# Kernel optimization log

Hardware: AMD Instinct MI355X
Metric: run time of the kernel (lower is better)

## Reference

```python
import jax, jax.numpy as jnp
import numpy as np

B, S, H = 4, 2048, 1024
E, F = 8, 4096
K = 2  # hardcoded top-k in the original forward


def setup_inputs() -> dict:
    key = jax.random.key(0)
    ks = jax.random.split(key, 8)
    scale = 0.02
    x = jax.random.normal(ks[0], (B, S, H), dtype=jnp.float32)
    Wr = jax.random.normal(ks[1], (H, E), dtype=jnp.float32) * scale
    br = jnp.zeros((E,), dtype=jnp.float32)
    W1 = jax.random.normal(ks[2], (E, H, F), dtype=jnp.float32) * scale
    b1 = jnp.zeros((E, F), dtype=jnp.float32)
    W2 = jax.random.normal(ks[3], (E, F, H), dtype=jnp.float32) * scale
    b2 = jnp.zeros((E, H), dtype=jnp.float32)
    return {"x": x, "Wr": Wr, "br": br, "W1": W1, "b1": b1, "W2": W2, "b2": b2}


def reference(x, Wr, br, W1, b1, W2, b2):
    # Router: [B,S,H] @ [H,E] -> [B,S,E]
    router_logits = jnp.einsum('bsh,he->bse', x, Wr) + br
    router_probs = jax.nn.softmax(router_logits, axis=-1)
    top_k_probs, top_k_indices = jax.lax.top_k(router_probs, K)
    top_k_probs = top_k_probs / jnp.sum(top_k_probs, axis=-1, keepdims=True)
    # NOTE: original code weights EVERY selected expert by the normalized top-1 prob.
    p0 = top_k_probs[..., 0]  # [B,S]

    combined = jnp.zeros((B, S, H), dtype=x.dtype)
    for e in range(E):
        mask = jnp.any(top_k_indices == e, axis=-1)  # [B,S]
        # Dense FFN (dropout deterministic => identity); gelu approximate (flax default)
        h = jax.nn.gelu(jnp.einsum('bsh,hf->bsf', x, W1[e]) + b1[e])
        y = jnp.einsum('bsf,fh->bsh', h, W2[e]) + b2[e]
        combined = combined + jnp.where(mask[..., None], y * p0[..., None], 0.0)
    return combined
```

## Files before the change

kernel.cpp:

```cpp
#include <hip/hip_runtime.h>
#include <hip/hip_bf16.h>


typedef __bf16 bf16;
typedef __attribute__((ext_vector_type(4))) __bf16 bf16x4;
typedef __attribute__((ext_vector_type(8))) __bf16 bf16x8;
typedef __attribute__((ext_vector_type(4))) float f32x4;

#define GLD16(g, l) __builtin_amdgcn_global_load_lds( \
    (__attribute__((address_space(1))) void*)(g),      \
    (__attribute__((address_space(3))) void*)(l), 16, 0, 0)

__device__ __forceinline__ float gelu_fast(float v) {
  float u = v * fmaf(v * v, 0.0713548162726f, 1.5957691216057308f);
  return v * __builtin_amdgcn_rcpf(1.0f + __expf(-u));
}

__global__ __launch_bounds__(256) void router_kernel(
    const float* __restrict__ x, const float* __restrict__ Wr,
    const float* __restrict__ br, int* __restrict__ e01,
    float* __restrict__ p0arr) {
  int wv = threadIdx.x >> 6;
  int l = threadIdx.x & 63;
  int t = blockIdx.x * 4 + wv;
  float acc[8];
#pragma unroll
  for (int e = 0; e < 8; e++) acc[e] = 0.f;
  const float* xr = x + (size_t)t * 1024;
#pragma unroll
  for (int i = 0; i < 16; i++) {
    int h = l + i * 64;
    float xv = xr[h];
    const float4* w4 = (const float4*)(Wr + h * 8);
    float4 wa = w4[0], wb = w4[1];
    acc[0] += xv * wa.x; acc[1] += xv * wa.y; acc[2] += xv * wa.z; acc[3] += xv * wa.w;
    acc[4] += xv * wb.x; acc[5] += xv * wb.y; acc[6] += xv * wb.z; acc[7] += xv * wb.w;
  }
#pragma unroll
  for (int e = 0; e < 8; e++) {
    float v = acc[e];
#pragma unroll
    for (int m = 1; m < 64; m <<= 1) v += __shfl_xor(v, m, 64);
    acc[e] = v + br[e];
  }
  int i1 = 0; float m1 = acc[0];
#pragma unroll
  for (int e = 1; e < 8; e++) { if (acc[e] > m1) { m1 = acc[e]; i1 = e; } }
  int i2 = -1; float m2 = -3.4e38f;
#pragma unroll
  for (int e = 0; e < 8; e++) { if (e != i1 && acc[e] > m2) { m2 = acc[e]; i2 = e; } }
  if (l == 0) {
    e01[t] = i1 | (i2 << 8);
    p0arr[t] = 1.0f / (1.0f + __expf(m2 - m1));
  }
}

__global__ __launch_bounds__(1024) void slots_kernel(
    const int* __restrict__ e01, int* __restrict__ off,
    int* __restrict__ slot1, int* __restrict__ slot2) {
  __shared__ int wtot[16];
  int tid = threadIdx.x;
  int l = tid & 63, wv = tid >> 6;
  int t0 = tid * 8;
  int i1[8], i2[8];
#pragma unroll
  for (int i = 0; i < 8; i++) {
    int ee = e01[t0 + i];
    i1[i] = ee & 255;
    i2[i] = (ee >> 8) & 255;
  }
  int running = 0;
  for (int e = 0; e < 8; e++) {
    int cthread = 0;
#pragma unroll
    for (int i = 0; i < 8; i++) cthread += (i1[i] == e) + (i2[i] == e);
    int inc = cthread;
#pragma unroll
    for (int d = 1; d < 64; d <<= 1) {
      int v = __shfl_up(inc, d, 64);
      if (l >= d) inc += v;
    }
    if (l == 63) wtot[wv] = inc;
    __syncthreads();
    int wbase = 0, total = 0;
#pragma unroll
    for (int w = 0; w < 16; w++) {
      int tw = wtot[w];
      wbase += (w < wv) ? tw : 0;
      total += tw;
    }
    int base = running + wbase + (inc - cthread);
#pragma unroll
    for (int i = 0; i < 8; i++) {
      if (i1[i] == e) { slot1[t0 + i] = base; base++; }
      if (i2[i] == e) { slot2[t0 + i] = base; base++; }
    }
    if (tid == 0) off[e] = running;
    running += (total + 127) & ~127;
    __syncthreads();
  }
  if (tid == 0) off[8] = running;
}

__global__ __launch_bounds__(256) void gather_kernel(
    const float* __restrict__ x, const int* __restrict__ slot1,
    const int* __restrict__ slot2, bf16* __restrict__ Xg) {
  int t = blockIdx.x;
  int s1 = slot1[t], s2 = slot2[t];
  float4 v = ((const float4*)(x + (size_t)t * 1024))[threadIdx.x];
  bf16x4 bv = { (bf16)v.x, (bf16)v.y, (bf16)v.z, (bf16)v.w };
  *(bf16x4*)(Xg + (size_t)s1 * 1024 + threadIdx.x * 4) = bv;
  *(bf16x4*)(Xg + (size_t)s2 * 1024 + threadIdx.x * 4) = bv;
}

__global__ __launch_bounds__(256) void tconv_kernel(
    const float* __restrict__ in, bf16* __restrict__ out, int R, int C) {
  __shared__ float tile[64][65];
  size_t base = (size_t)blockIdx.z * R * C;
  int gr0 = blockIdx.y * 64, gc0 = blockIdx.x * 64;
#pragma unroll
  for (int i = 0; i < 16; i++) {
    int idx = threadIdx.x + i * 256;
    int r = idx >> 6, c = idx & 63;
    tile[r][c] = in[base + (size_t)(gr0 + r) * C + gc0 + c];
  }
  __syncthreads();
  int rr0 = (threadIdx.x & 15) * 4;
#pragma unroll
  for (int i = 0; i < 4; i++) {
    int cc = (threadIdx.x >> 4) + i * 16;
    bf16x4 v = { (bf16)tile[rr0][cc], (bf16)tile[rr0 + 1][cc],
                 (bf16)tile[rr0 + 2][cc], (bf16)tile[rr0 + 3][cc] };
    *(bf16x4*)&out[base + (size_t)(gc0 + cc) * R + gr0 + rr0] = v;
  }
}

__device__ __forceinline__ void gemm8_mainloop(
    const bf16* __restrict__ Abase, const bf16* __restrict__ Bbase,
    int K, char* smem, f32x4 acc[4][4], int wr, int wc, int l) {
  const int NT = K >> 6;
  int tid = threadIdx.x;
  size_t K2 = (size_t)K * 2;
  const char* sA0; const char* sA1;
  const char* sB0; const char* sB1; const char* sB2; const char* sB3;
  {
    int p0 = tid * 16, r0 = p0 >> 7, c0 = p0 & 127;
    int p1 = p0 + 8192, r1 = p1 >> 7, c1 = p1 & 127;
    int p2 = p0 + 16384, r2 = p2 >> 7, c2 = p2 & 127;
    int p3 = p0 + 24576, r3 = p3 >> 7, c3 = p3 & 127;
    sA0 = (const char*)Abase + (size_t)r0 * K2 + (c0 ^ ((r0 & 7) << 4));
    sA1 = (const char*)Abase + (size_t)r1 * K2 + (c1 ^ ((r1 & 7) << 4));
    sB0 = (const char*)Bbase + (size_t)r0 * K2 + (c0 ^ ((r0 & 7) << 4));
    sB1 = (const char*)Bbase + (size_t)r1 * K2 + (c1 ^ ((r1 & 7) << 4));
    sB2 = (const char*)Bbase + (size_t)r2 * K2 + (c2 ^ ((r2 & 7) << 4));
    sB3 = (const char*)Bbase + (size_t)r3 * K2 + (c3 ^ ((r3 & 7) << 4));
  }
  const int dA = tid * 16;
  const int dB = 16384 + tid * 16;
  int offA[4], offBf[4];
#pragma unroll
  for (int t = 0; t < 4; t++) {
    int ra = wr * 64 + t * 16 + (l & 15);
    offA[t] = ra * 128 + ((((l >> 4) << 4)) ^ ((ra & 7) << 4));
    int rb = wc * 64 + t * 16 + (l & 15);
    offBf[t] = 16384 + rb * 128 + ((((l >> 4) << 4)) ^ ((rb & 7) << 4));
  }
#pragma unroll
  for (int t = 0; t < 2; t++) {
    char* bu = smem + t * 49152;
    GLD16(sA0 + t * 128, bu + dA);
    GLD16(sA1 + t * 128, bu + dA + 8192);
    GLD16(sB0 + t * 128, bu + dB);
    GLD16(sB1 + t * 128, bu + dB + 8192);
    GLD16(sB2 + t * 128, bu + dB + 16384);
    GLD16(sB3 + t * 128, bu + dB + 24576);
  }
  sA0 += 256; sA1 += 256; sB0 += 256; sB1 += 256; sB2 += 256; sB3 += 256;
  asm volatile("s_waitcnt vmcnt(6)" ::: "memory");
  __builtin_amdgcn_s_barrier();
  char* bc = smem;
  char* bn2 = smem + 2 * 49152;
  for (int kt = 0; kt < NT; kt++) {
    bool st = (kt + 2) < NT;
    bf16x8 af[4], bfv[4];
#pragma unroll
    for (int t = 0; t < 4; t++) {
      af[t] = *(const bf16x8*)(bc + offA[t]);
      bfv[t] = *(const bf16x8*)(bc + offBf[t]);
    }
    if (st) {
      GLD16(sA0, bn2 + dA);
      GLD16(sA1, bn2 + dA + 8192);
      GLD16(sB0, bn2 + dB);
    }
    __builtin_amdgcn_s_barrier();
    asm volatile("s_waitcnt lgkmcnt(0)" ::: "memory");
    __builtin_amdgcn_s_setprio(1);
#pragma unroll
    for (int mf = 0; mf < 4; mf++)
#pragma unroll
      for (int nf = 0; nf < 4; nf++)
        acc[mf][nf] = __builtin_amdgcn_mfma_f32_16x16x32_bf16(bfv[nf], af[mf], acc[mf][nf], 0, 0, 0);
    __builtin_amdgcn_s_setprio(0);
    __builtin_amdgcn_s_barrier();
#pragma unroll
    for (int t = 0; t < 4; t++) {
      af[t] = *(const bf16x8*)(bc + (offA[t] ^ 64));
      bfv[t] = *(const bf16x8*)(bc + (offBf[t] ^ 64));
    }
    if (st) {
      GLD16(sB1, bn2 + dB + 8192);
      GLD16(sB2, bn2 + dB + 16384);
      GLD16(sB3, bn2 + dB + 24576);
      sA0 += 128; sA1 += 128; sB0 += 128; sB1 += 128; sB2 += 128; sB3 += 128;
    }
    __builtin_amdgcn_s_barrier();
    asm volatile("s_waitcnt lgkmcnt(0)" ::: "memory");
    __builtin_amdgcn_s_setprio(1);
#pragma unroll
    for (int mf = 0; mf < 4; mf++)
#pragma unroll
      for (int nf = 0; nf < 4; nf++)
        acc[mf][nf] = __builtin_amdgcn_mfma_f32_16x16x32_bf16(bfv[nf], af[mf], acc[mf][nf], 0, 0, 0);
    __builtin_amdgcn_s_setprio(0);
    if (st) {
      asm volatile("s_waitcnt vmcnt(6)" ::: "memory");
    } else if (kt + 1 < NT) {
      asm volatile("s_waitcnt vmcnt(0)" ::: "memory");
    }
    __builtin_amdgcn_s_barrier();
    bc += 49152; if (bc == smem + 147456) bc = smem;
    bn2 += 49152; if (bn2 == smem + 147456) bn2 = smem;
  }
}

__global__ __launch_bounds__(512) void gemm1_kernel(
    const bf16* __restrict__ Xg, const bf16* __restrict__ W1t,
    const float* __restrict__ b1, bf16* __restrict__ hbuf,
    const int* __restrict__ off) {
  __shared__ __align__(16) char smem[147456];
  int b = blockIdx.x;
  int xcd = b & 7, j = b >> 3;
  int m_tile = xcd * 17 + (j >> 4);
  int n_tile = j & 15;
  int row0 = m_tile * 128;
  if (row0 >= off[8]) return;
  int e = 0;
#pragma unroll
  for (int i = 0; i < 8; i++) { if (row0 >= off[i + 1]) e = i + 1; }
  int tid = threadIdx.x;
  int w = tid >> 6, l = tid & 63;
  int wr = w >> 2, wc = w & 3;
  f32x4 acc[4][4];
#pragma unroll
  for (int a = 0; a < 4; a++)
#pragma unroll
    for (int bb = 0; bb < 4; bb++) acc[a][bb] = (f32x4){0.f, 0.f, 0.f, 0.f};
  gemm8_mainloop(Xg + (size_t)row0 * 1024,
                 W1t + ((size_t)e * 4096 + n_tile * 256) * 1024,
                 1024, smem, acc, wr, wc, l);
  int mrow = l & 15, nq = (l >> 4) * 4;
  int gn0 = n_tile * 256 + wc * 64 + nq;
  f32x4 bv[4];
#pragma unroll
  for (int nf = 0; nf < 4; nf++)
    bv[nf] = *(const f32x4*)(b1 + e * 4096 + gn0 + nf * 16);
#pragma unroll
  for (int mf = 0; mf < 4; mf++) {
    int gm = row0 + wr * 64 + mf * 16 + mrow;
    bf16* rp = hbuf + (size_t)gm * 4096 + gn0;
#pragma unroll
    for (int nf = 0; nf < 4; nf++) {
      bf16x4 o;
#pragma unroll
      for (int jj = 0; jj < 4; jj++)
        o[jj] = (bf16)gelu_fast(acc[mf][nf][jj] + bv[nf][jj]);
      *(bf16x4*)(rp + nf * 16) = o;
    }
  }
}

__global__ __launch_bounds__(512) void gemm2_kernel(
    const bf16* __restrict__ hbuf, const bf16* __restrict__ W2t,
    const float* __restrict__ b2, bf16* __restrict__ yb,
    const int* __restrict__ off) {
  __shared__ __align__(16) char smem[147456];
  int b = blockIdx.x;
  int xcd = b & 7, j = b >> 3;
  int m_tile = xcd * 17 + (j >> 2);
  int n_tile = j & 3;
  int row0 = m_tile * 128;
  if (row0 >= off[8]) return;
  int e = 0;
#pragma unroll
  for (int i = 0; i < 8; i++) { if (row0 >= off[i + 1]) e = i + 1; }
  int tid = threadIdx.x;
  int w = tid >> 6, l = tid & 63;
  int wr = w >> 2, wc = w & 3;
  f32x4 acc[4][4];
#pragma unroll
  for (int a = 0; a < 4; a++)
#pragma unroll
    for (int bb = 0; bb < 4; bb++) acc[a][bb] = (f32x4){0.f, 0.f, 0.f, 0.f};
  gemm8_mainloop(hbuf + (size_t)row0 * 4096,
                 W2t + ((size_t)e * 1024 + n_tile * 256) * 4096,
                 4096, smem, acc, wr, wc, l);
  int mrow = l & 15, nq = (l >> 4) * 4;
  int gn0 = n_tile * 256 + wc * 64 + nq;
  f32x4 bv[4];
#pragma unroll
  for (int nf = 0; nf < 4; nf++)
    bv[nf] = *(const f32x4*)(b2 + e * 1024 + gn0 + nf * 16);
#pragma unroll
  for (int mf = 0; mf < 4; mf++) {
    int gm = row0 + wr * 64 + mf * 16 + mrow;
    bf16* rp = yb + (size_t)gm * 1024 + gn0;
#pragma unroll
    for (int nf = 0; nf < 4; nf++) {
      bf16x4 o;
#pragma unroll
      for (int jj = 0; jj < 4; jj++)
        o[jj] = (bf16)(acc[mf][nf][jj] + bv[nf][jj]);
      *(bf16x4*)(rp + nf * 16) = o;
    }
  }
}

__global__ __launch_bounds__(256) void combine_kernel(
    const bf16* __restrict__ yb, const int* __restrict__ slot1,
    const int* __restrict__ slot2, const float* __restrict__ p0arr,
    float* __restrict__ out) {
  int t = blockIdx.x;
  int s1 = slot1[t], s2 = slot2[t];
  float w0 = p0arr[t];
  bf16x4 a = *(const bf16x4*)(yb + (size_t)s1 * 1024 + threadIdx.x * 4);
  bf16x4 b = *(const bf16x4*)(yb + (size_t)s2 * 1024 + threadIdx.x * 4);
  float4 o;
  o.x = w0 * ((float)a[0] + (float)b[0]);
  o.y = w0 * ((float)a[1] + (float)b[1]);
  o.z = w0 * ((float)a[2] + (float)b[2]);
  o.w = w0 * ((float)a[3] + (float)b[3]);
  *(float4*)(out + (size_t)t * 1024 + threadIdx.x * 4) = o;
}

extern "C" void kernel_launch(void* const* d_in, const int* in_sizes, int n_in,
                              void* d_out, int out_size, void* d_ws, size_t ws_size,
                              hipStream_t stream) {
  const float* x  = (const float*)d_in[0];
  const float* Wr = (const float*)d_in[1];
  const float* br = (const float*)d_in[2];
  const float* W1 = (const float*)d_in[3];
  const float* b1 = (const float*)d_in[4];
  const float* W2 = (const float*)d_in[5];
  const float* b2 = (const float*)d_in[6];
  float* out = (float*)d_out;

  char* ws = (char*)d_ws;
  int*   off   = (int*)(ws + 0);
  int*   e01   = (int*)(ws + 256);
  float* p0    = (float*)(ws + 33024);
  int*   slot1 = (int*)(ws + 65792);
  int*   slot2 = (int*)(ws + 98560);
  bf16*  Xg    = (bf16*)(ws + 131584);
  bf16*  W1t   = (bf16*)(ws + 35783168ULL);
  bf16*  W2t   = (bf16*)(ws + 102892032ULL);
  bf16*  hb    = (bf16*)(ws + 170000896ULL);
  bf16*  yb    = Xg;

  tconv_kernel<<<dim3(64, 16, 8), 256, 0, stream>>>(W1, W1t, 1024, 4096);
  tconv_kernel<<<dim3(16, 64, 8), 256, 0, stream>>>(W2, W2t, 4096, 1024);
  router_kernel<<<2048, 256, 0, stream>>>(x, Wr, br, e01, p0);
  slots_kernel<<<1, 1024, 0, stream>>>(e01, off, slot1, slot2);
  gather_kernel<<<8192, 256, 0, stream>>>(x, slot1, slot2, Xg);
  gemm1_kernel<<<2176, 512, 0, stream>>>(Xg, W1t, b1, hb, off);
  gemm2_kernel<<<544, 512, 0, stream>>>(hb, W2t, b2, yb, off);
  combine_kernel<<<8192, 256, 0, stream>>>(yb, slot1, slot2, p0, out);
}
```

Before: 758.2 us.

## Use 256x256 expert GEMM tiles with per-expert tile list and 4-stage pipeline

Replaces the 128x256 GEMM tile with a 256x256 tile (8x4 MFMA fragments per wave) using a 64-wide K step and a 4-buffer, 3-ahead global-to-LDS prefetch ring. Experts are no longer padded to 128 rows. The slots kernel builds a compact list of 256-row tiles, each tagged with its expert, and the GEMMs mask stores past the expert's row end. Bigger tiles raise arithmetic intensity and halve the block count, at the cost of more accumulator registers and wasted MFMA work on partial tiles. The launch bounds request two blocks per CU.

```diff
diff --git a/kernel.cpp b/kernel.cpp
--- a/kernel.cpp
+++ b/kernel.cpp
@@ -56,7 +56,7 @@
 }
 
 __global__ __launch_bounds__(1024) void slots_kernel(
-    const int* __restrict__ e01, int* __restrict__ off,
+    const int* __restrict__ e01, int* __restrict__ meta,
     int* __restrict__ slot1, int* __restrict__ slot2) {
   __shared__ int wtot[16];
   int tid = threadIdx.x;
@@ -69,8 +69,10 @@
     i1[i] = ee & 255;
     i2[i] = (ee >> 8) & 255;
   }
+  int offl[9];
   int running = 0;
   for (int e = 0; e < 8; e++) {
+    offl[e] = running;
     int cthread = 0;
 #pragma unroll
     for (int i = 0; i < 8; i++) cthread += (i1[i] == e) + (i2[i] == e);
@@ -95,11 +97,19 @@
       if (i1[i] == e) { slot1[t0 + i] = base; base++; }
       if (i2[i] == e) { slot2[t0 + i] = base; base++; }
     }
-    if (tid == 0) off[e] = running;
-    running += (total + 127) & ~127;
+    running += total;
     __syncthreads();
   }
-  if (tid == 0) off[8] = running;
+  offl[8] = running;
+  if (tid == 0) {
+#pragma unroll
+    for (int e = 0; e < 9; e++) meta[e] = offl[e];
+    int nt = 0;
+    for (int e = 0; e < 8; e++)
+      for (int r = offl[e]; r < offl[e + 1]; r += 256)
+        meta[16 + (nt++)] = r | (e << 20);
+    meta[10] = nt;
+  }
 }
 
 __global__ __launch_bounds__(256) void gather_kernel(
@@ -135,63 +145,60 @@
   }
 }
 
-__device__ __forceinline__ void gemm8_mainloop(
+__device__ __forceinline__ void gemm256_core(
     const bf16* __restrict__ Abase, const bf16* __restrict__ Bbase,
-    int K, char* smem, f32x4 acc[4][4], int wr, int wc, int l) {
-  const int NT = K >> 6;
+    int K, int NT, char* smem, f32x4 acc[8][4], int wr, int wc, int l) {
   int tid = threadIdx.x;
   size_t K2 = (size_t)K * 2;
-  const char* sA0; const char* sA1;
-  const char* sB0; const char* sB1; const char* sB2; const char* sB3;
-  {
-    int p0 = tid * 16, r0 = p0 >> 7, c0 = p0 & 127;
-    int p1 = p0 + 8192, r1 = p1 >> 7, c1 = p1 & 127;
-    int p2 = p0 + 16384, r2 = p2 >> 7, c2 = p2 & 127;
-    int p3 = p0 + 24576, r3 = p3 >> 7, c3 = p3 & 127;
-    sA0 = (const char*)Abase + (size_t)r0 * K2 + (c0 ^ ((r0 & 7) << 4));
-    sA1 = (const char*)Abase + (size_t)r1 * K2 + (c1 ^ ((r1 & 7) << 4));
-    sB0 = (const char*)Bbase + (size_t)r0 * K2 + (c0 ^ ((r0 & 7) << 4));
-    sB1 = (const char*)Bbase + (size_t)r1 * K2 + (c1 ^ ((r1 & 7) << 4));
-    sB2 = (const char*)Bbase + (size_t)r2 * K2 + (c2 ^ ((r2 & 7) << 4));
-    sB3 = (const char*)Bbase + (size_t)r3 * K2 + (c3 ^ ((r3 & 7) << 4));
-  }
-  const int dA = tid * 16;
-  const int dB = 16384 + tid * 16;
-  int offA[4], offBf[4];
-#pragma unroll
-  for (int t = 0; t < 4; t++) {
-    int ra = wr * 64 + t * 16 + (l & 15);
-    offA[t] = ra * 128 + ((((l >> 4) << 4)) ^ ((ra & 7) << 4));
-    int rb = wc * 64 + t * 16 + (l & 15);
-    offBf[t] = 16384 + rb * 128 + ((((l >> 4) << 4)) ^ ((rb & 7) << 4));
-  }
-#pragma unroll
-  for (int t = 0; t < 2; t++) {
-    char* bu = smem + t * 49152;
-    GLD16(sA0 + t * 128, bu + dA);
-    GLD16(sA1 + t * 128, bu + dA + 8192);
-    GLD16(sB0 + t * 128, bu + dB);
-    GLD16(sB1 + t * 128, bu + dB + 8192);
-    GLD16(sB2 + t * 128, bu + dB + 16384);
-    GLD16(sB3 + t * 128, bu + dB + 24576);
-  }
-  sA0 += 256; sA1 += 256; sB0 += 256; sB1 += 256; sB2 += 256; sB3 += 256;
-  asm volatile("s_waitcnt vmcnt(6)" ::: "memory");
+  const char* src[4];
+  int dst[4];
+#pragma unroll
+  for (int i = 0; i < 4; i++) {
+    int s = (i & 1) ? (tid + 512) : tid;
+    int byteoff = s * 16;
+    int p = byteoff >> 7;
+    int W = byteoff & 127;
+    int L = W ^ ((p & 7) << 4);
+    int r = 2 * p + (L >> 6);
+    int c = L & 63;
+    const char* base = (const char*)((i >= 2) ? Bbase : Abase);
+    src[i] = base + (size_t)r * K2 + c;
+    dst[i] = ((i >= 2) ? 16384 : 0) + byteoff;
+  }
+  int offA[8], offB[4];
+  int kc16 = (l >> 4) << 4;
+#pragma unroll
+  for (int mf = 0; mf < 8; mf++) {
+    int r = wr * 128 + mf * 16 + (l & 15);
+    int p = r >> 1;
+    offA[mf] = (p << 7) + ((((r & 1) << 6) | kc16) ^ ((p & 7) << 4));
+  }
+#pragma unroll
+  for (int nf = 0; nf < 4; nf++) {
+    int r = wc * 64 + nf * 16 + (l & 15);
+    int p = r >> 1;
+    offB[nf] = 16384 + (p << 7) + ((((r & 1) << 6) | kc16) ^ ((p & 7) << 4));
+  }
+#pragma unroll
+  for (int t = 0; t < 3; t++) {
+    char* bu = smem + t * 32768;
+#pragma unroll
+    for (int i = 0; i < 4; i++) GLD16(src[i] + t * 64, bu + dst[i]);
+  }
+  asm volatile("s_waitcnt vmcnt(8)" ::: "memory");
   __builtin_amdgcn_s_barrier();
-  char* bc = smem;
-  char* bn2 = smem + 2 * 49152;
-  for (int kt = 0; kt < NT; kt++) {
-    bool st = (kt + 2) < NT;
-    bf16x8 af[4], bfv[4];
-#pragma unroll
-    for (int t = 0; t < 4; t++) {
-      af[t] = *(const bf16x8*)(bc + offA[t]);
-      bfv[t] = *(const bf16x8*)(bc + offBf[t]);
-    }
+  for (int t = 0; t < NT; t++) {
+    char* bc = smem + (t & 3) * 32768;
+    char* bs = smem + ((t + 3) & 3) * 32768;
+    bool st = (t + 3) < NT;
+    bf16x8 bfr[4], af[4];
+#pragma unroll
+    for (int nf = 0; nf < 4; nf++) bfr[nf] = *(const bf16x8*)(bc + offB[nf]);
+#pragma unroll
+    for (int mf = 0; mf < 4; mf++) af[mf] = *(const bf16x8*)(bc + offA[mf]);
     if (st) {
-      GLD16(sA0, bn2 + dA);
-      GLD16(sA1, bn2 + dA + 8192);
-      GLD16(sB0, bn2 + dB);
+      GLD16(src[0] + (t + 3) * 64, bs + dst[0]);
+      GLD16(src[1] + (t + 3) * 64, bs + dst[1]);
     }
     __builtin_amdgcn_s_barrier();
     asm volatile("s_waitcnt lgkmcnt(0)" ::: "memory");
@@ -200,19 +207,14 @@
     for (int mf = 0; mf < 4; mf++)
 #pragma unroll
       for (int nf = 0; nf < 4; nf++)
-        acc[mf][nf] = __builtin_amdgcn_mfma_f32_16x16x32_bf16(bfv[nf], af[mf], acc[mf][nf], 0, 0, 0);
+        acc[mf][nf] = __builtin_amdgcn_mfma_f32_16x16x32_bf16(bfr[nf], af[mf], acc[mf][nf], 0, 0, 0);
     __builtin_amdgcn_s_setprio(0);
     __builtin_amdgcn_s_barrier();
 #pragma unroll
-    for (int t = 0; t < 4; t++) {
-      af[t] = *(const bf16x8*)(bc + (offA[t] ^ 64));
-      bfv[t] = *(const bf16x8*)(bc + (offBf[t] ^ 64));
-    }
+    for (int mf = 0; mf < 4; mf++) af[mf] = *(const bf16x8*)(bc + offA[mf + 4]);
     if (st) {
-      GLD16(sB1, bn2 + dB + 8192);
-      GLD16(sB2, bn2 + dB + 16384);
-      GLD16(sB3, bn2 + dB + 24576);
-      sA0 += 128; sA1 += 128; sB0 += 128; sB1 += 128; sB2 += 128; sB3 += 128;
+      GLD16(src[2] + (t + 3) * 64, bs + dst[2]);
+      GLD16(src[3] + (t + 3) * 64, bs + dst[3]);
     }
     __builtin_amdgcn_s_barrier();
     asm volatile("s_waitcnt lgkmcnt(0)" ::: "memory");
@@ -221,44 +223,40 @@
     for (int mf = 0; mf < 4; mf++)
 #pragma unroll
       for (int nf = 0; nf < 4; nf++)
-        acc[mf][nf] = __builtin_amdgcn_mfma_f32_16x16x32_bf16(bfv[nf], af[mf], acc[mf][nf], 0, 0, 0);
+        acc[mf + 4][nf] = __builtin_amdgcn_mfma_f32_16x16x32_bf16(bfr[nf], af[mf], acc[mf + 4][nf], 0, 0, 0);
     __builtin_amdgcn_s_setprio(0);
-    if (st) {
-      asm volatile("s_waitcnt vmcnt(6)" ::: "memory");
-    } else if (kt + 1 < NT) {
-      asm volatile("s_waitcnt vmcnt(0)" ::: "memory");
-    }
+    if ((t + 3) < NT)      { asm volatile("s_waitcnt vmcnt(8)" ::: "memory"); }
+    else if ((t + 2) < NT) { asm volatile("s_waitcnt vmcnt(4)" ::: "memory"); }
+    else if ((t + 1) < NT) { asm volatile("s_waitcnt vmcnt(0)" ::: "memory"); }
     __builtin_amdgcn_s_barrier();
-    bc += 49152; if (bc == smem + 147456) bc = smem;
-    bn2 += 49152; if (bn2 == smem + 147456) bn2 = smem;
-  }
-}
-
-__global__ __launch_bounds__(512) void gemm1_kernel(
+  }
+}
+
+__global__ __launch_bounds__(512, 2) void gemm1_kernel(
     const bf16* __restrict__ Xg, const bf16* __restrict__ W1t,
     const float* __restrict__ b1, bf16* __restrict__ hbuf,
-    const int* __restrict__ off) {
-  __shared__ __align__(16) char smem[147456];
+    const int* __restrict__ meta) {
+  __shared__ __align__(16) char smem[131072];
   int b = blockIdx.x;
   int xcd = b & 7, j = b >> 3;
-  int m_tile = xcd * 17 + (j >> 4);
+  int m_idx = (j >> 4) * 8 + xcd;
   int n_tile = j & 15;
-  int row0 = m_tile * 128;
-  if (row0 >= off[8]) return;
-  int e = 0;
-#pragma unroll
-  for (int i = 0; i < 8; i++) { if (row0 >= off[i + 1]) e = i + 1; }
+  if (m_idx >= meta[10]) return;
+  int ti = meta[16 + m_idx];
+  int row0 = ti & 0xFFFFF;
+  int e = ti >> 20;
+  int rowEnd = meta[1 + e];
   int tid = threadIdx.x;
   int w = tid >> 6, l = tid & 63;
   int wr = w >> 2, wc = w & 3;
-  f32x4 acc[4][4];
-#pragma unroll
-  for (int a = 0; a < 4; a++)
+  f32x4 acc[8][4];
+#pragma unroll
+  for (int a = 0; a < 8; a++)
 #pragma unroll
     for (int bb = 0; bb < 4; bb++) acc[a][bb] = (f32x4){0.f, 0.f, 0.f, 0.f};
-  gemm8_mainloop(Xg + (size_t)row0 * 1024,
-                 W1t + ((size_t)e * 4096 + n_tile * 256) * 1024,
-                 1024, smem, acc, wr, wc, l);
+  gemm256_core(Xg + (size_t)row0 * 1024,
+               W1t + ((size_t)e * 4096 + n_tile * 256) * 1024,
+               1024, 32, smem, acc, wr, wc, l);
   int mrow = l & 15, nq = (l >> 4) * 4;
   int gn0 = n_tile * 256 + wc * 64 + nq;
   f32x4 bv[4];
@@ -266,45 +264,47 @@
   for (int nf = 0; nf < 4; nf++)
     bv[nf] = *(const f32x4*)(b1 + e * 4096 + gn0 + nf * 16);
 #pragma unroll
-  for (int mf = 0; mf < 4; mf++) {
-    int gm = row0 + wr * 64 + mf * 16 + mrow;
-    bf16* rp = hbuf + (size_t)gm * 4096 + gn0;
-#pragma unroll
-    for (int nf = 0; nf < 4; nf++) {
-      bf16x4 o;
-#pragma unroll
-      for (int jj = 0; jj < 4; jj++)
-        o[jj] = (bf16)gelu_fast(acc[mf][nf][jj] + bv[nf][jj]);
-      *(bf16x4*)(rp + nf * 16) = o;
-    }
-  }
-}
-
-__global__ __launch_bounds__(512) void gemm2_kernel(
+  for (int mf = 0; mf < 8; mf++) {
+    int gm = row0 + wr * 128 + mf * 16 + mrow;
+    if (gm < rowEnd) {
+      bf16* rp = hbuf + (size_t)gm * 4096 + gn0;
+#pragma unroll
+      for (int nf = 0; nf < 4; nf++) {
+        bf16x4 o;
+#pragma unroll
+        for (int jj = 0; jj < 4; jj++)
+          o[jj] = (bf16)gelu_fast(acc[mf][nf][jj] + bv[nf][jj]);
+        *(bf16x4*)(rp + nf * 16) = o;
+      }
+    }
+  }
+}
+
+__global__ __launch_bounds__(512, 2) void gemm2_kernel(
     const bf16* __restrict__ hbuf, const bf16* __restrict__ W2t,
     const float* __restrict__ b2, bf16* __restrict__ yb,
-    const int* __restrict__ off) {
-  __shared__ __align__(16) char smem[147456];
+    const int* __restrict__ meta) {
+  __shared__ __align__(16) char smem[131072];
   int b = blockIdx.x;
   int xcd = b & 7, j = b >> 3;
-  int m_tile = xcd * 17 + (j >> 2);
+  int m_idx = (j >> 2) * 8 + xcd;
   int n_tile = j & 3;
-  int row0 = m_tile * 128;
-  if (row0 >= off[8]) return;
-  int e = 0;
-#pragma unroll
-  for (int i = 0; i < 8; i++) { if (row0 >= off[i + 1]) e = i + 1; }
+  if (m_idx >= meta[10]) return;
+  int ti = meta[16 + m_idx];
+  int row0 = ti & 0xFFFFF;
+  int e = ti >> 20;
+  int rowEnd = meta[1 + e];
   int tid = threadIdx.x;
   int w = tid >> 6, l = tid & 63;
   int wr = w >> 2, wc = w & 3;
-  f32x4 acc[4][4];
-#pragma unroll
-  for (int a = 0; a < 4; a++)
+  f32x4 acc[8][4];
+#pragma unroll
+  for (int a = 0; a < 8; a++)
 #pragma unroll
     for (int bb = 0; bb < 4; bb++) acc[a][bb] = (f32x4){0.f, 0.f, 0.f, 0.f};
-  gemm8_mainloop(hbuf + (size_t)row0 * 4096,
-                 W2t + ((size_t)e * 1024 + n_tile * 256) * 4096,
-                 4096, smem, acc, wr, wc, l);
+  gemm256_core(hbuf + (size_t)row0 * 4096,
+               W2t + ((size_t)e * 1024 + n_tile * 256) * 4096,
+               4096, 128, smem, acc, wr, wc, l);
   int mrow = l & 15, nq = (l >> 4) * 4;
   int gn0 = n_tile * 256 + wc * 64 + nq;
   f32x4 bv[4];
@@ -312,16 +312,18 @@
   for (int nf = 0; nf < 4; nf++)
     bv[nf] = *(const f32x4*)(b2 + e * 1024 + gn0 + nf * 16);
 #pragma unroll
-  for (int mf = 0; mf < 4; mf++) {
-    int gm = row0 + wr * 64 + mf * 16 + mrow;
-    bf16* rp = yb + (size_t)gm * 1024 + gn0;
-#pragma unroll
-    for (int nf = 0; nf < 4; nf++) {
-      bf16x4 o;
-#pragma unroll
-      for (int jj = 0; jj < 4; jj++)
-        o[jj] = (bf16)(acc[mf][nf][jj] + bv[nf][jj]);
-      *(bf16x4*)(rp + nf * 16) = o;
+  for (int mf = 0; mf < 8; mf++) {
+    int gm = row0 + wr * 128 + mf * 16 + mrow;
+    if (gm < rowEnd) {
+      bf16* rp = yb + (size_t)gm * 1024 + gn0;
+#pragma unroll
+      for (int nf = 0; nf < 4; nf++) {
+        bf16x4 o;
+#pragma unroll
+        for (int jj = 0; jj < 4; jj++)
+          o[jj] = (bf16)(acc[mf][nf][jj] + bv[nf][jj]);
+        *(bf16x4*)(rp + nf * 16) = o;
+      }
     }
   }
 }
@@ -356,23 +358,23 @@
   float* out = (float*)d_out;
 
   char* ws = (char*)d_ws;
-  int*   off   = (int*)(ws + 0);
-  int*   e01   = (int*)(ws + 256);
-  float* p0    = (float*)(ws + 33024);
-  int*   slot1 = (int*)(ws + 65792);
-  int*   slot2 = (int*)(ws + 98560);
-  bf16*  Xg    = (bf16*)(ws + 131584);
-  bf16*  W1t   = (bf16*)(ws + 35783168ULL);
-  bf16*  W2t   = (bf16*)(ws + 102892032ULL);
-  bf16*  hb    = (bf16*)(ws + 170000896ULL);
+  int*   meta  = (int*)(ws + 0);
+  int*   e01   = (int*)(ws + 4096);
+  float* p0    = (float*)(ws + 36864);
+  int*   slot1 = (int*)(ws + 69632);
+  int*   slot2 = (int*)(ws + 102400);
+  bf16*  Xg    = (bf16*)(ws + 135168);
+  bf16*  W1t   = (bf16*)(ws + 34213888ULL);
+  bf16*  W2t   = (bf16*)(ws + 101322752ULL);
+  bf16*  hb    = (bf16*)(ws + 168431616ULL);
   bf16*  yb    = Xg;
 
   tconv_kernel<<<dim3(64, 16, 8), 256, 0, stream>>>(W1, W1t, 1024, 4096);
   tconv_kernel<<<dim3(16, 64, 8), 256, 0, stream>>>(W2, W2t, 4096, 1024);
   router_kernel<<<2048, 256, 0, stream>>>(x, Wr, br, e01, p0);
-  slots_kernel<<<1, 1024, 0, stream>>>(e01, off, slot1, slot2);
+  slots_kernel<<<1, 1024, 0, stream>>>(e01, meta, slot1, slot2);
   gather_kernel<<<8192, 256, 0, stream>>>(x, slot1, slot2, Xg);
-  gemm1_kernel<<<2176, 512, 0, stream>>>(Xg, W1t, b1, hb, off);
-  gemm2_kernel<<<544, 512, 0, stream>>>(hb, W2t, b2, yb, off);
+  gemm1_kernel<<<1152, 512, 0, stream>>>(Xg, W1t, b1, hb, meta);
+  gemm2_kernel<<<288, 512, 0, stream>>>(hb, W2t, b2, yb, meta);
   combine_kernel<<<8192, 256, 0, stream>>>(yb, slot1, slot2, p0, out);
 }
```

Result: slower. 792.6 us (+4.5%).
